# Kernel tuning notes

Hardware: AMD Instinct MI355X
Metric: run time of the kernel (lower is better)

## Reference

```python
import jax, jax.numpy as jnp
import numpy as np

B, S, E, H = 4, 2048, 1024, 16
D = E // H  # head_size = 64

def setup_inputs() -> dict:
    key = jax.random.key(0)
    k1, k2, k3 = jax.random.split(key, 3)
    x = jax.random.normal(k1, (B, S, E), dtype=jnp.float32)
    # torch Linear weight is (out,in); we store transposed (in,out) for x @ W
    w_attn = jax.random.normal(k2, (E, 3 * E), dtype=jnp.float32) * (1.0 / np.sqrt(E))
    w_proj = jax.random.normal(k3, (E, E), dtype=jnp.float32) * (1.0 / np.sqrt(E))
    return {"x": x, "w_attn": w_attn, "w_proj": w_proj}

def reference(x, w_attn, w_proj):
    b, s, e = x.shape
    qkv = x @ w_attn                      # (B,S,3E)
    q, k, v = jnp.split(qkv, 3, axis=2)
    # (B,S,H,D) -> (B,H,S,D)
    q = q.reshape(b, s, H, D).transpose(0, 2, 1, 3)
    k = k.reshape(b, s, H, D).transpose(0, 2, 1, 3)
    v = v.reshape(b, s, H, D).transpose(0, 2, 1, 3)
    scale = 1.0 / np.sqrt(D).astype(np.float32)
    att = jnp.einsum('bhqd,bhkd->bhqk', q, k) * scale  # (B,H,S,S)
    causal = jnp.tril(jnp.ones((s, s), dtype=bool))
    att = jnp.where(causal[None, None, :, :], att, jnp.float32(-jnp.inf))
    att = jax.nn.softmax(att, axis=-1)
    # dropout layers are identity in eval mode
    y = jnp.einsum('bhqk,bhkd->bhqd', att, v)          # (B,H,S,D)
    y = y.transpose(0, 2, 1, 3).reshape(b, s, e)       # (B,S,E)
    return y @ w_proj
```

## Files before the change

kernel.cpp:

```cpp
#include <hip/hip_runtime.h>
#include <hip/hip_bf16.h>
#include <cstdint>

typedef __attribute__((ext_vector_type(8))) short bf16x8;
typedef __attribute__((ext_vector_type(4))) short short4v;
typedef __attribute__((ext_vector_type(4))) float f32x4;

#define MFMA(a, b, c) __builtin_amdgcn_mfma_f32_16x16x32_bf16((a), (b), (c), 0, 0, 0)

__device__ __forceinline__ unsigned short f2bf(float f) {
  union { float f; unsigned int u; } v;
  v.f = f;
  unsigned int r = v.u + 0x7FFFu + ((v.u >> 16) & 1u);
  return (unsigned short)(r >> 16);
}

__device__ __forceinline__ unsigned short f2bf_ru(float f) {
  union { float f; unsigned int u; } v;
  v.f = f;
  return (unsigned short)((v.u + 0x8000u) >> 16);
}

__device__ __forceinline__ void async_cp16(const unsigned short* g, unsigned short* l) {
  __builtin_amdgcn_global_load_lds(
      (const __attribute__((address_space(1))) unsigned int*)g,
      (__attribute__((address_space(3))) unsigned int*)l, 16, 0, 0);
}

__global__ __launch_bounds__(256) void cvt_x(const float* __restrict__ in,
                                             unsigned short* __restrict__ out) {
  size_t i = ((size_t)blockIdx.x * 256 + threadIdx.x) * 8;
  float4 a = *(const float4*)(in + i);
  float4 b = *(const float4*)(in + i + 4);
  bf16x8 p;
  p[0] = (short)f2bf(a.x); p[1] = (short)f2bf(a.y);
  p[2] = (short)f2bf(a.z); p[3] = (short)f2bf(a.w);
  p[4] = (short)f2bf(b.x); p[5] = (short)f2bf(b.y);
  p[6] = (short)f2bf(b.z); p[7] = (short)f2bf(b.w);
  *(bf16x8*)(out + i) = p;
}

__global__ __launch_bounds__(256) void transpose_cvt(const float* __restrict__ in,
                                                     unsigned short* __restrict__ out,
                                                     int K, int N) {
  __shared__ float tile[64][65];
  int k0 = blockIdx.x * 64;
  int n0 = blockIdx.y * 64;
  int c = threadIdx.x & 63;
  int rb = threadIdx.x >> 6;
#pragma unroll
  for (int i = 0; i < 16; ++i) {
    int r = rb * 16 + i;
    tile[r][c] = in[(size_t)(k0 + r) * N + (n0 + c)];
  }
  __syncthreads();
#pragma unroll
  for (int i = 0; i < 16; ++i) {
    int r = rb * 16 + i;
    out[(size_t)(n0 + r) * K + (k0 + c)] = f2bf(tile[c][r]);
  }
}

__global__ __launch_bounds__(256) void gemm_qkv(const unsigned short* __restrict__ X,
                                                const unsigned short* __restrict__ WT,
                                                unsigned short* __restrict__ qb,
                                                unsigned short* __restrict__ kb,
                                                unsigned short* __restrict__ vt) {
  const int K = 1024;
  __shared__ unsigned short As[128 * 64];
  __shared__ unsigned short Bs[128 * 64];
  int t = threadIdx.x, lane = t & 63, w = t >> 6;
  int quad = lane >> 4, l15 = lane & 15;
  int sl7 = l15 & 7;
  int wm = (w >> 1) * 64, wn = (w & 1) * 64;
  int row0 = blockIdx.y * 128, col0 = blockIdx.x * 128;
  int srow = w * 8 + (lane >> 3);
  int schunk = (lane & 7) ^ (lane >> 3);
  const unsigned short* aSrc = X + (size_t)(row0 + srow) * K + schunk * 8;
  const unsigned short* bSrc = WT + (size_t)(col0 + srow) * K + schunk * 8;
  unsigned short* ldsA = &As[(w * 8) * 64];
  unsigned short* ldsB = &Bs[(w * 8) * 64];
  f32x4 zero4 = {0.f, 0.f, 0.f, 0.f};
  f32x4 acc[4][4];
#pragma unroll
  for (int i = 0; i < 4; ++i)
#pragma unroll
    for (int j = 0; j < 4; ++j) acc[i][j] = zero4;

  for (int k0 = 0; k0 < K; k0 += 64) {
    __syncthreads();
#pragma unroll
    for (int i = 0; i < 4; ++i)
      async_cp16(aSrc + (size_t)i * 32 * K + k0, ldsA + i * 32 * 64);
#pragma unroll
    for (int i = 0; i < 4; ++i)
      async_cp16(bSrc + (size_t)i * 32 * K + k0, ldsB + i * 32 * 64);
    __syncthreads();
#pragma unroll
    for (int h = 0; h < 2; ++h) {
      bf16x8 af[4], bfr[4];
#pragma unroll
      for (int mt = 0; mt < 4; ++mt)
        af[mt] = *(const bf16x8*)&As[(wm + mt * 16 + l15) * 64 +
                                     ((h * 4 + quad) ^ sl7) * 8];
#pragma unroll
      for (int nt = 0; nt < 4; ++nt)
        bfr[nt] = *(const bf16x8*)&Bs[(wn + nt * 16 + l15) * 64 +
                                      ((h * 4 + quad) ^ sl7) * 8];
#pragma unroll
      for (int mt = 0; mt < 4; ++mt)
#pragma unroll
        for (int nt = 0; nt < 4; ++nt)
          acc[mt][nt] = MFMA(af[mt], bfr[nt], acc[mt][nt]);
    }
  }

  const float qscale = 0.125f * 1.4426950408889634f;
#pragma unroll
  for (int mt = 0; mt < 4; ++mt) {
    int rix0 = row0 + wm + mt * 16 + quad * 4;
    int b = rix0 >> 11;
    int s0 = rix0 & 2047;
#pragma unroll
    for (int nt = 0; nt < 4; ++nt) {
      int c = col0 + wn + nt * 16 + l15;
      int which = c >> 10;
      int e = c & 1023;
      int h = e >> 6, d = e & 63;
      size_t bh = (size_t)b * 16 + h;
      if (which == 2) {
        short4v pv;
#pragma unroll
        for (int r = 0; r < 4; ++r) pv[r] = (short)f2bf(acc[mt][nt][r]);
        *(short4v*)(vt + (bh * 64 + d) * 2048 + s0) = pv;
      } else {
        unsigned short* dst = (which == 0) ? qb : kb;
        float sc = (which == 0) ? qscale : 1.0f;
#pragma unroll
        for (int r = 0; r < 4; ++r)
          dst[(bh * 2048 + (s0 + r)) * 64 + d] = f2bf(acc[mt][nt][r] * sc);
      }
    }
  }
}

__global__ __launch_bounds__(256, 2) void flash_attn(const unsigned short* __restrict__ qb,
                                                     const unsigned short* __restrict__ kb,
                                                     const unsigned short* __restrict__ vt,
                                                     unsigned short* __restrict__ yb) {
  __shared__ unsigned short Ks[64 * 68];
  __shared__ unsigned short P[4][16 * 68];
  int idx = blockIdx.x;
  int bh = idx & 63;
  int p = idx >> 6;
  int t = threadIdx.x, lane = t & 63, w = t >> 6;
  int quad = lane >> 4, l15 = lane & 15;
  unsigned short* Pw = P[w];
  f32x4 zero4 = {0.f, 0.f, 0.f, 0.f};
  bf16x8 ones;
#pragma unroll
  for (int i = 0; i < 8; ++i) ones[i] = (short)0x3F80;

  int srow = t >> 2;
  int sseg = (t & 3) * 8;
  const unsigned short* Kg = kb + ((size_t)bh * 2048 + srow) * 64 + sseg;
  int b = bh >> 4, h = bh & 15;

  for (int seg = 0; seg < 2; ++seg) {
    int qt = seg ? p : (15 - p);
    int qrow0 = qt * 128 + w * 32;
    int ktmax = 2 * qt + 1;

    bf16x8 aq0[2], aq1[2];
#pragma unroll
    for (int s = 0; s < 2; ++s) {
      const unsigned short* Qp =
          qb + ((size_t)bh * 2048 + qrow0 + s * 16 + l15) * 64 + quad * 8;
      aq0[s] = *(const bf16x8*)Qp;
      aq1[s] = *(const bf16x8*)(Qp + 32);
    }
    f32x4 o[2][4], accl[2];
#pragma unroll
    for (int s = 0; s < 2; ++s) {
      accl[s] = zero4;
#pragma unroll
      for (int nt = 0; nt < 4; ++nt) o[s][nt] = zero4;
    }

    bf16x8 kg0 = *(const bf16x8*)Kg;
    bf16x8 kg1 = *(const bf16x8*)(Kg + 32);

    for (int kt = 0; kt <= ktmax; ++kt) {
      int kbase = kt * 64;
      __syncthreads();
      *(bf16x8*)&Ks[srow * 68 + sseg] = kg0;
      *(bf16x8*)&Ks[srow * 68 + sseg + 32] = kg1;
      __syncthreads();
      if (kt < ktmax) {
        const unsigned short* nk = Kg + (size_t)(kbase + 64) * 64;
        kg0 = *(const bf16x8*)nk;
        kg1 = *(const bf16x8*)(nk + 32);
      }
      if (kbase > qrow0 + 31) continue;

      bf16x8 vf0[4], vf1[4];
#pragma unroll
      for (int nt = 0; nt < 4; ++nt) {
        const unsigned short* Vp =
            vt + ((size_t)bh * 64 + nt * 16 + l15) * 2048 + kbase + quad * 8;
        vf0[nt] = *(const bf16x8*)Vp;
        vf1[nt] = *(const bf16x8*)(Vp + 32);
      }
      bf16x8 kf0[4], kf1[4];
#pragma unroll
      for (int nt = 0; nt < 4; ++nt) {
        kf0[nt] = *(const bf16x8*)&Ks[(nt * 16 + l15) * 68 + quad * 8];
        kf1[nt] = *(const bf16x8*)&Ks[(nt * 16 + l15) * 68 + 32 + quad * 8];
      }

#pragma unroll
      for (int s = 0; s < 2; ++s) {
        int rowb = qrow0 + s * 16;
        if (kbase > rowb + 15) continue;
        f32x4 sv[4];
#pragma unroll
        for (int nt = 0; nt < 4; ++nt) {
          f32x4 z = zero4;
          z = MFMA(aq0[s], kf0[nt], z);
          z = MFMA(aq1[s], kf1[nt], z);
          sv[nt] = z;
        }
        if (kbase + 63 > rowb) {
#pragma unroll
          for (int nt = 0; nt < 4; ++nt) {
            int col = kbase + nt * 16 + l15;
#pragma unroll
            for (int r = 0; r < 4; ++r)
              if (col > rowb + quad * 4 + r) sv[nt][r] = -1e30f;
          }
        }
#pragma unroll
        for (int nt = 0; nt < 4; ++nt)
#pragma unroll
          for (int r = 0; r < 4; ++r) {
            float pv = __builtin_amdgcn_exp2f(sv[nt][r]);
            Pw[(quad * 4 + r) * 68 + nt * 16 + l15] = f2bf_ru(pv);
          }
        bf16x8 ap0 = *(const bf16x8*)&Pw[l15 * 68 + quad * 8];
        bf16x8 ap1 = *(const bf16x8*)&Pw[l15 * 68 + 32 + quad * 8];
        accl[s] = MFMA(ap0, ones, accl[s]);
        accl[s] = MFMA(ap1, ones, accl[s]);
#pragma unroll
        for (int nt = 0; nt < 4; ++nt) {
          o[s][nt] = MFMA(ap0, vf0[nt], o[s][nt]);
          o[s][nt] = MFMA(ap1, vf1[nt], o[s][nt]);
        }
      }
    }

#pragma unroll
    for (int s = 0; s < 2; ++s) {
      float inv[4];
#pragma unroll
      for (int r = 0; r < 4; ++r) inv[r] = 1.0f / accl[s][r];
#pragma unroll
      for (int nt = 0; nt < 4; ++nt) {
        int e = h * 64 + nt * 16 + l15;
#pragma unroll
        for (int r = 0; r < 4; ++r) {
          int srow_g = qrow0 + s * 16 + quad * 4 + r;
          yb[((size_t)b * 2048 + srow_g) * 1024 + e] = f2bf(o[s][nt][r] * inv[r]);
        }
      }
    }
  }
}

__global__ __launch_bounds__(256) void gemm_proj(const unsigned short* __restrict__ Y,
                                                 const unsigned short* __restrict__ WT,
                                                 float* __restrict__ out) {
  const int K = 1024;
  __shared__ unsigned short As[128 * 64];
  __shared__ unsigned short Bs[128 * 64];
  int t = threadIdx.x, lane = t & 63, w = t >> 6;
  int quad = lane >> 4, l15 = lane & 15;
  int sl7 = l15 & 7;
  int wm = (w >> 1) * 64, wn = (w & 1) * 64;
  int row0 = blockIdx.y * 128, col0 = blockIdx.x * 128;
  int srow = w * 8 + (lane >> 3);
  int schunk = (lane & 7) ^ (lane >> 3);
  const unsigned short* aSrc = Y + (size_t)(row0 + srow) * K + schunk * 8;
  const unsigned short* bSrc = WT + (size_t)(col0 + srow) * K + schunk * 8;
  unsigned short* ldsA = &As[(w * 8) * 64];
  unsigned short* ldsB = &Bs[(w * 8) * 64];
  f32x4 zero4 = {0.f, 0.f, 0.f, 0.f};
  f32x4 acc[4][4];
#pragma unroll
  for (int i = 0; i < 4; ++i)
#pragma unroll
    for (int j = 0; j < 4; ++j) acc[i][j] = zero4;

  for (int k0 = 0; k0 < K; k0 += 64) {
    __syncthreads();
#pragma unroll
    for (int i = 0; i < 4; ++i)
      async_cp16(aSrc + (size_t)i * 32 * K + k0, ldsA + i * 32 * 64);
#pragma unroll
    for (int i = 0; i < 4; ++i)
      async_cp16(bSrc + (size_t)i * 32 * K + k0, ldsB + i * 32 * 64);
    __syncthreads();
#pragma unroll
    for (int h = 0; h < 2; ++h) {
      bf16x8 af[4], bfr[4];
#pragma unroll
      for (int mt = 0; mt < 4; ++mt)
        af[mt] = *(const bf16x8*)&As[(wm + mt * 16 + l15) * 64 +
                                     ((h * 4 + quad) ^ sl7) * 8];
#pragma unroll
      for (int nt = 0; nt < 4; ++nt)
        bfr[nt] = *(const bf16x8*)&Bs[(wn + nt * 16 + l15) * 64 +
                                      ((h * 4 + quad) ^ sl7) * 8];
#pragma unroll
      for (int mt = 0; mt < 4; ++mt)
#pragma unroll
        for (int nt = 0; nt < 4; ++nt)
          acc[mt][nt] = MFMA(af[mt], bfr[nt], acc[mt][nt]);
    }
  }

#pragma unroll
  for (int mt = 0; mt < 4; ++mt) {
    int rix0 = row0 + wm + mt * 16 + quad * 4;
#pragma unroll
    for (int nt = 0; nt < 4; ++nt) {
      int c = col0 + wn + nt * 16 + l15;
#pragma unroll
      for (int r = 0; r < 4; ++r)
        out[(size_t)(rix0 + r) * 1024 + c] = acc[mt][nt][r];
    }
  }
}

extern "C" void kernel_launch(void* const* d_in, const int* in_sizes, int n_in,
                              void* d_out, int out_size, void* d_ws, size_t ws_size,
                              hipStream_t stream) {
  const float* x = (const float*)d_in[0];
  const float* w_attn = (const float*)d_in[1];
  const float* w_proj = (const float*)d_in[2];
  float* out = (float*)d_out;
  char* ws = (char*)d_ws;
  unsigned short* wT  = (unsigned short*)(ws + 0);
  unsigned short* wpT = (unsigned short*)(ws + 6291456);
  unsigned short* qb  = (unsigned short*)(ws + 8388608);
  unsigned short* kb  = (unsigned short*)(ws + 25165824);
  unsigned short* vt  = (unsigned short*)(ws + 41943040);
  unsigned short* xyb = (unsigned short*)(ws + 58720256);

  cvt_x<<<4096, 256, 0, stream>>>(x, xyb);
  transpose_cvt<<<dim3(16, 48), 256, 0, stream>>>(w_attn, wT, 1024, 3072);
  transpose_cvt<<<dim3(16, 16), 256, 0, stream>>>(w_proj, wpT, 1024, 1024);
  gemm_qkv<<<dim3(24, 64), 256, 0, stream>>>(xyb, wT, qb, kb, vt);
  flash_attn<<<dim3(512), 256, 0, stream>>>(qb, kb, vt, xyb);
  gemm_proj<<<dim3(8, 64), 256, 0, stream>>>(xyb, wpT, out);
}
```

Baseline: 262.2 us.

## Double-buffer K tiles via async LDS loads and launch one query tile per block

The flash attention kernel no longer pairs two query tiles per block for causal balance. It launches 1024 blocks, one per query tile, heaviest tiles first, and raises the occupancy hint to 4 blocks per CU. K tiles are now loaded into a double-buffered, XOR-swizzled LDS buffer with async global-to-LDS copies, which removes one barrier per iteration and the register staging. The trade-off is a larger LDS footprint and possible register pressure, plus reliance on the scheduler to balance uneven per-block work.

Result: slower. 415.2 us (+58.4%).

```diff
diff --git a/kernel.cpp b/kernel.cpp
--- a/kernel.cpp
+++ b/kernel.cpp
@@ -144,133 +144,133 @@
   }
 }
 
-__global__ __launch_bounds__(256, 2) void flash_attn(const unsigned short* __restrict__ qb,
+__global__ __launch_bounds__(256, 4) void flash_attn(const unsigned short* __restrict__ qb,
                                                      const unsigned short* __restrict__ kb,
                                                      const unsigned short* __restrict__ vt,
                                                      unsigned short* __restrict__ yb) {
-  __shared__ unsigned short Ks[64 * 68];
+  __shared__ unsigned short Ks[2][64 * 64];
   __shared__ unsigned short P[4][16 * 68];
   int idx = blockIdx.x;
   int bh = idx & 63;
-  int p = idx >> 6;
+  int qt = 15 - (idx >> 6);
   int t = threadIdx.x, lane = t & 63, w = t >> 6;
   int quad = lane >> 4, l15 = lane & 15;
+  int sl7 = l15 & 7;
+  int qrow0 = qt * 128 + w * 32;
+  int ktmax = 2 * qt + 1;
   unsigned short* Pw = P[w];
   f32x4 zero4 = {0.f, 0.f, 0.f, 0.f};
   bf16x8 ones;
 #pragma unroll
   for (int i = 0; i < 8; ++i) ones[i] = (short)0x3F80;
-
-  int srow = t >> 2;
-  int sseg = (t & 3) * 8;
-  const unsigned short* Kg = kb + ((size_t)bh * 2048 + srow) * 64 + sseg;
   int b = bh >> 4, h = bh & 15;
 
-  for (int seg = 0; seg < 2; ++seg) {
-    int qt = seg ? p : (15 - p);
-    int qrow0 = qt * 128 + w * 32;
-    int ktmax = 2 * qt + 1;
-
-    bf16x8 aq0[2], aq1[2];
+  bf16x8 aq0[2], aq1[2];
+#pragma unroll
+  for (int s = 0; s < 2; ++s) {
+    const unsigned short* Qp =
+        qb + ((size_t)bh * 2048 + qrow0 + s * 16 + l15) * 64 + quad * 8;
+    aq0[s] = *(const bf16x8*)Qp;
+    aq1[s] = *(const bf16x8*)(Qp + 32);
+  }
+  f32x4 o[2][4], accl[2];
+#pragma unroll
+  for (int s = 0; s < 2; ++s) {
+    accl[s] = zero4;
+#pragma unroll
+    for (int nt = 0; nt < 4; ++nt) o[s][nt] = zero4;
+  }
+
+  int srow = w * 8 + (lane >> 3);
+  int schunk = (lane & 7) ^ (lane >> 3);
+  const unsigned short* Kg = kb + (size_t)bh * 2048 * 64;
+  const unsigned short* Vbase = vt + (size_t)bh * 64 * 2048;
+
+  {
+    const unsigned short* s0 = Kg + (size_t)srow * 64 + schunk * 8;
+    async_cp16(s0, &Ks[0][(w * 8) * 64]);
+    async_cp16(s0 + 32 * 64, &Ks[0][(w * 8 + 32) * 64]);
+  }
+
+  for (int kt = 0; kt <= ktmax; ++kt) {
+    int kbase = kt * 64;
+    __syncthreads();
+    if (kt < ktmax) {
+      const unsigned short* sn = Kg + (size_t)(kbase + 64 + srow) * 64 + schunk * 8;
+      unsigned short* dn = &Ks[(kt + 1) & 1][0];
+      async_cp16(sn, dn + (w * 8) * 64);
+      async_cp16(sn + 32 * 64, dn + (w * 8 + 32) * 64);
+    }
+    if (kbase > qrow0 + 31) continue;
+
+    const unsigned short* ksb = &Ks[kt & 1][0];
+    bf16x8 vf0[4], vf1[4];
+#pragma unroll
+    for (int nt = 0; nt < 4; ++nt) {
+      const unsigned short* Vp =
+          Vbase + (size_t)(nt * 16 + l15) * 2048 + kbase + quad * 8;
+      vf0[nt] = *(const bf16x8*)Vp;
+      vf1[nt] = *(const bf16x8*)(Vp + 32);
+    }
+    bf16x8 kf0[4], kf1[4];
+#pragma unroll
+    for (int nt = 0; nt < 4; ++nt) {
+      kf0[nt] = *(const bf16x8*)&ksb[(nt * 16 + l15) * 64 + ((quad ^ sl7) * 8)];
+      kf1[nt] = *(const bf16x8*)&ksb[(nt * 16 + l15) * 64 + (((4 + quad) ^ sl7) * 8)];
+    }
+
 #pragma unroll
     for (int s = 0; s < 2; ++s) {
-      const unsigned short* Qp =
-          qb + ((size_t)bh * 2048 + qrow0 + s * 16 + l15) * 64 + quad * 8;
-      aq0[s] = *(const bf16x8*)Qp;
-      aq1[s] = *(const bf16x8*)(Qp + 32);
-    }
-    f32x4 o[2][4], accl[2];
-#pragma unroll
-    for (int s = 0; s < 2; ++s) {
-      accl[s] = zero4;
-#pragma unroll
-      for (int nt = 0; nt < 4; ++nt) o[s][nt] = zero4;
-    }
-
-    bf16x8 kg0 = *(const bf16x8*)Kg;
-    bf16x8 kg1 = *(const bf16x8*)(Kg + 32);
-
-    for (int kt = 0; kt <= ktmax; ++kt) {
-      int kbase = kt * 64;
-      __syncthreads();
-      *(bf16x8*)&Ks[srow * 68 + sseg] = kg0;
-      *(bf16x8*)&Ks[srow * 68 + sseg + 32] = kg1;
-      __syncthreads();
-      if (kt < ktmax) {
-        const unsigned short* nk = Kg + (size_t)(kbase + 64) * 64;
-        kg0 = *(const bf16x8*)nk;
-        kg1 = *(const bf16x8*)(nk + 32);
-      }
-      if (kbase > qrow0 + 31) continue;
-
-      bf16x8 vf0[4], vf1[4];
+      int rowb = qrow0 + s * 16;
+      if (kbase > rowb + 15) continue;
+      f32x4 sv[4];
 #pragma unroll
       for (int nt = 0; nt < 4; ++nt) {
-        const unsigned short* Vp =
-            vt + ((size_t)bh * 64 + nt * 16 + l15) * 2048 + kbase + quad * 8;
-        vf0[nt] = *(const bf16x8*)Vp;
-        vf1[nt] = *(const bf16x8*)(Vp + 32);
-      }
-      bf16x8 kf0[4], kf1[4];
+        f32x4 z = zero4;
+        z = MFMA(aq0[s], kf0[nt], z);
+        z = MFMA(aq1[s], kf1[nt], z);
+        sv[nt] = z;
+      }
+      if (kbase + 63 > rowb) {
+#pragma unroll
+        for (int nt = 0; nt < 4; ++nt) {
+          int col = kbase + nt * 16 + l15;
+#pragma unroll
+          for (int r = 0; r < 4; ++r)
+            if (col > rowb + quad * 4 + r) sv[nt][r] = -1e30f;
+        }
+      }
+#pragma unroll
+      for (int nt = 0; nt < 4; ++nt)
+#pragma unroll
+        for (int r = 0; r < 4; ++r) {
+          float pv = __builtin_amdgcn_exp2f(sv[nt][r]);
+          Pw[(quad * 4 + r) * 68 + nt * 16 + l15] = f2bf_ru(pv);
+        }
+      bf16x8 ap0 = *(const bf16x8*)&Pw[l15 * 68 + quad * 8];
+      bf16x8 ap1 = *(const bf16x8*)&Pw[l15 * 68 + 32 + quad * 8];
+      accl[s] = MFMA(ap0, ones, accl[s]);
+      accl[s] = MFMA(ap1, ones, accl[s]);
 #pragma unroll
       for (int nt = 0; nt < 4; ++nt) {
-        kf0[nt] = *(const bf16x8*)&Ks[(nt * 16 + l15) * 68 + quad * 8];
-        kf1[nt] = *(const bf16x8*)&Ks[(nt * 16 + l15) * 68 + 32 + quad * 8];
-      }
-
-#pragma unroll
-      for (int s = 0; s < 2; ++s) {
-        int rowb = qrow0 + s * 16;
-        if (kbase > rowb + 15) continue;
-        f32x4 sv[4];
-#pragma unroll
-        for (int nt = 0; nt < 4; ++nt) {
-          f32x4 z = zero4;
-          z = MFMA(aq0[s], kf0[nt], z);
-          z = MFMA(aq1[s], kf1[nt], z);
-          sv[nt] = z;
-        }
-        if (kbase + 63 > rowb) {
-#pragma unroll
-          for (int nt = 0; nt < 4; ++nt) {
-            int col = kbase + nt * 16 + l15;
-#pragma unroll
-            for (int r = 0; r < 4; ++r)
-              if (col > rowb + quad * 4 + r) sv[nt][r] = -1e30f;
-          }
-        }
-#pragma unroll
-        for (int nt = 0; nt < 4; ++nt)
-#pragma unroll
-          for (int r = 0; r < 4; ++r) {
-            float pv = __builtin_amdgcn_exp2f(sv[nt][r]);
-            Pw[(quad * 4 + r) * 68 + nt * 16 + l15] = f2bf_ru(pv);
-          }
-        bf16x8 ap0 = *(const bf16x8*)&Pw[l15 * 68 + quad * 8];
-        bf16x8 ap1 = *(const bf16x8*)&Pw[l15 * 68 + 32 + quad * 8];
-        accl[s] = MFMA(ap0, ones, accl[s]);
-        accl[s] = MFMA(ap1, ones, accl[s]);
-#pragma unroll
-        for (int nt = 0; nt < 4; ++nt) {
-          o[s][nt] = MFMA(ap0, vf0[nt], o[s][nt]);
-          o[s][nt] = MFMA(ap1, vf1[nt], o[s][nt]);
-        }
-      }
-    }
-
-#pragma unroll
-    for (int s = 0; s < 2; ++s) {
-      float inv[4];
-#pragma unroll
-      for (int r = 0; r < 4; ++r) inv[r] = 1.0f / accl[s][r];
-#pragma unroll
-      for (int nt = 0; nt < 4; ++nt) {
-        int e = h * 64 + nt * 16 + l15;
-#pragma unroll
-        for (int r = 0; r < 4; ++r) {
-          int srow_g = qrow0 + s * 16 + quad * 4 + r;
-          yb[((size_t)b * 2048 + srow_g) * 1024 + e] = f2bf(o[s][nt][r] * inv[r]);
-        }
+        o[s][nt] = MFMA(ap0, vf0[nt], o[s][nt]);
+        o[s][nt] = MFMA(ap1, vf1[nt], o[s][nt]);
+      }
+    }
+  }
+
+#pragma unroll
+  for (int s = 0; s < 2; ++s) {
+    float inv[4];
+#pragma unroll
+    for (int r = 0; r < 4; ++r) inv[r] = 1.0f / accl[s][r];
+#pragma unroll
+    for (int nt = 0; nt < 4; ++nt) {
+      int e = h * 64 + nt * 16 + l15;
+#pragma unroll
+      for (int r = 0; r < 4; ++r) {
+        int srow_g = qrow0 + s * 16 + quad * 4 + r;
+        yb[((size_t)b * 2048 + srow_g) * 1024 + e] = f2bf(o[s][nt][r] * inv[r]);
       }
     }
   }
@@ -360,6 +360,6 @@
   transpose_cvt<<<dim3(16, 48), 256, 0, stream>>>(w_attn, wT, 1024, 3072);
   transpose_cvt<<<dim3(16, 16), 256, 0, stream>>>(w_proj, wpT, 1024, 1024);
   gemm_qkv<<<dim3(24, 64), 256, 0, stream>>>(xyb, wT, qb, kb, vt);
-  flash_attn<<<dim3(512), 256, 0, stream>>>(qb, kb, vt, xyb);
+  flash_attn<<<dim3(1024), 256, 0, stream>>>(qb, kb, vt, xyb);
   gemm_proj<<<dim3(8, 64), 256, 0, stream>>>(xyb, wpT, out);
 }
```
